# Optimization experiments

Measured on AMD Instinct MI355X. Metric: run time of the kernel, lower is better.

The kernel has to match this reference:

```python
import jax, jax.numpy as jnp
import numpy as np
from jax import lax

FEAT_STRIDE = 16
SCALES = np.array([8.0, 16.0, 32.0])
RATIOS = np.array([0.5, 1.0, 2.0])
PRE_NMS_TOPN = 6000
POST_NMS_TOPN = 300
NMS_THRESH = 0.7


def _whctrs(a):
    w = a[2] - a[0] + 1.0
    h = a[3] - a[1] + 1.0
    return w, h, a[0] + 0.5 * (w - 1.0), a[1] + 0.5 * (h - 1.0)


def _mkanchors(ws, hs, xc, yc):
    return np.stack([xc - 0.5 * (ws - 1.0), yc - 0.5 * (hs - 1.0),
                     xc + 0.5 * (ws - 1.0), yc + 0.5 * (hs - 1.0)], axis=1)


def generate_anchors(base_size=16):
    base = np.array([0.0, 0.0, base_size - 1.0, base_size - 1.0])
    w, h, xc, yc = _whctrs(base)
    size = w * h
    ws = np.round(np.sqrt(size / RATIOS))
    hs = np.round(ws * RATIOS)
    ratio_anchors = _mkanchors(ws, hs, np.full_like(ws, xc), np.full_like(ws, yc))
    out = []
    for a in ratio_anchors:
        w, h, xc, yc = _whctrs(a)
        out.append(_mkanchors(w * SCALES, h * SCALES,
                              np.full_like(SCALES, xc), np.full_like(SCALES, yc)))
    return np.concatenate(out, axis=0).astype(np.float32)  # (A=9, 4)


def _pairwise_iou(boxes):
    x1, y1, x2, y2 = boxes[:, 0], boxes[:, 1], boxes[:, 2], boxes[:, 3]
    area = (x2 - x1 + 1.0) * (y2 - y1 + 1.0)
    iw = jnp.maximum(0.0, jnp.minimum(x2[:, None], x2[None, :]) - jnp.maximum(x1[:, None], x1[None, :]) + 1.0)
    ih = jnp.maximum(0.0, jnp.minimum(y2[:, None], y2[None, :]) - jnp.maximum(y1[:, None], y1[None, :]) + 1.0)
    inter = iw * ih
    return inter / (area[:, None] + area[None, :] - inter)


def _nms_keep(iou, thresh):
    n = iou.shape[0]
    idx = jnp.arange(n)
    def body(keep, i):
        suppress = keep[i] & (iou[i] > thresh) & (idx > i)
        return keep & (~suppress), None
    keep, _ = lax.scan(body, jnp.ones((n,), dtype=bool), idx)
    return keep


def _per_image(props, sc):
    # descending score sort, keep top pre_nms
    order = jnp.argsort(-sc)[:PRE_NMS_TOPN]
    boxes = props[order]  # (PRE, 4)
    iou = _pairwise_iou(boxes)  # (PRE, PRE)
    keep = _nms_keep(iou, NMS_THRESH)
    rank = jnp.cumsum(keep) - 1
    valid = keep & (rank < POST_NMS_TOPN)
    slot = jnp.where(valid, rank, POST_NMS_TOPN)  # dump invalid into spare slot
    out = jnp.zeros((POST_NMS_TOPN + 1, 4), boxes.dtype)
    out = out.at[slot].set(jnp.where(valid[:, None], boxes, 0.0))
    return out[:POST_NMS_TOPN]


def reference(scores, bbox_deltas, im_info):
    B, C2, H, W = scores.shape
    A = C2 // 2
    anchors = jnp.asarray(generate_anchors())  # (A, 4)
    sx = (jnp.arange(W) * FEAT_STRIDE).astype(jnp.float32)
    sy = (jnp.arange(H) * FEAT_STRIDE).astype(jnp.float32)
    gy, gx = jnp.meshgrid(sy, sx, indexing='ij')
    shifts = jnp.stack([gx.ravel(), gy.ravel(), gx.ravel(), gy.ravel()], axis=1)  # (K, 4)
    all_anchors = (anchors[None, :, :] + shifts[:, None, :]).reshape(-1, 4)  # (K*A, 4)

    deltas = bbox_deltas.transpose(0, 2, 3, 1).reshape(B, -1, 4)  # (B, K*A, 4)
    sc = scores[:, A:].transpose(0, 2, 3, 1).reshape(B, -1)        # (B, K*A)

    # bbox_transform_inv
    wa = all_anchors[:, 2] - all_anchors[:, 0] + 1.0
    ha = all_anchors[:, 3] - all_anchors[:, 1] + 1.0
    cxa = all_anchors[:, 0] + 0.5 * wa
    cya = all_anchors[:, 1] + 0.5 * ha
    dx, dy, dw, dh = deltas[..., 0], deltas[..., 1], deltas[..., 2], deltas[..., 3]
    pcx = dx * wa + cxa
    pcy = dy * ha + cya
    pw = jnp.exp(dw) * wa
    ph = jnp.exp(dh) * ha
    x1 = pcx - 0.5 * pw
    y1 = pcy - 0.5 * ph
    x2 = pcx + 0.5 * pw
    y2 = pcy + 0.5 * ph

    # clip_boxes
    im_h = im_info[:, 0:1]
    im_w = im_info[:, 1:2]
    x1 = jnp.clip(x1, 0.0, im_w - 1.0)
    x2 = jnp.clip(x2, 0.0, im_w - 1.0)
    y1 = jnp.clip(y1, 0.0, im_h - 1.0)
    y2 = jnp.clip(y2, 0.0, im_h - 1.0)
    props = jnp.stack([x1, y1, x2, y2], axis=-1)  # (B, K*A, 4)

    out_boxes = jax.vmap(_per_image)(props, sc)  # (B, POST, 4)
    batch_idx = jnp.broadcast_to(
        jnp.arange(B, dtype=out_boxes.dtype)[:, None, None], (B, POST_NMS_TOPN, 1))
    return jnp.concatenate([batch_idx, out_boxes], axis=-1)  # (B, POST, 5)


def setup_inputs() -> dict:
    key = jax.random.key(0)
    k1, k2 = jax.random.split(key)
    B, A, H, W = 4, 9, 50, 76
    scores = jax.random.uniform(k1, (B, 2 * A, H, W), dtype=jnp.float32)
    bbox_deltas = jax.random.normal(k2, (B, 4 * A, H, W), dtype=jnp.float32) * 0.1
    im_info = jnp.ones((B, 3), jnp.float32) * jnp.array([800.0, 1216.0, 1.0], jnp.float32)
    return {"scores": scores, "bbox_deltas": bbox_deltas, "im_info": im_info}
```

## Files before the change

kernel.cpp:

```cpp
#include <hip/hip_runtime.h>
#include <stdint.h>

#define B_     4
#define A_     9
#define H_     50
#define W_     76
#define HW_    (H_ * W_)
#define N_     (HW_ * A_)
#define PRE_   6000
#define POST_  300
#define NBIN   16384
#define BINOFF 0xC000
#define SKCAP  8192
#define ACTMAX 256
#define FXCAP  2048
#define NB_    94

__constant__ float c_anchors[9][4] = {
    { -84.f,  -40.f,  99.f,  55.f},
    {-176.f,  -88.f, 191.f, 103.f},
    {-360.f, -184.f, 375.f, 199.f},
    { -56.f,  -56.f,  71.f,  71.f},
    {-120.f, -120.f, 135.f, 135.f},
    {-248.f, -248.f, 263.f, 263.f},
    { -36.f,  -80.f,  51.f,  95.f},
    { -80.f, -168.f,  95.f, 183.f},
    {-168.f, -344.f, 183.f, 359.f},
};

__device__ __forceinline__ int sb_bin(unsigned int sb) {
    int bin = (int)((~sb) >> 16) - BINOFF;
    return bin < 0 ? 0 : bin;
}

__global__ __launch_bounds__(1024) void k_hp(const float* __restrict__ scores,
                                             unsigned int* __restrict__ hist,
                                             unsigned int* __restrict__ prefw,
                                             unsigned int* __restrict__ actA,
                                             unsigned int* __restrict__ actB,
                                             unsigned int* __restrict__ actcnt) {
    int b = blockIdx.x, tid = threadIdx.x;
    int lane = tid & 63, wid = tid >> 6;
    __shared__ unsigned int s_hist[NBIN];
    __shared__ unsigned int s_ws[64];
    __shared__ unsigned int s_aA[ACTMAX];
    __shared__ unsigned int s_aB[ACTMAX];
    __shared__ int s_actn;
    if (tid == 0) s_actn = 0;
    for (int i = tid; i < NBIN; i += 1024) s_hist[i] = 0u;
    __syncthreads();

    const float* sc = scores + (size_t)((b * 2 * A_) + A_) * HW_;
    for (int i = tid; i < N_; i += 1024) {
        unsigned int sb = __float_as_uint(sc[i]);
        atomicAdd(&s_hist[sb_bin(sb)], 1u);
    }
    __syncthreads();

    uint4* h4 = (uint4*)(hist + b * NBIN);
    uint4* p4 = (uint4*)(prefw + b * NBIN);
    const uint4* s4 = (const uint4*)s_hist;
    uint4 c[4];
    unsigned int tsum[4], inc[4];
#pragma unroll
    for (int p = 0; p < 4; ++p) {
        c[p] = s4[p * 1024 + tid];
        tsum[p] = c[p].x + c[p].y + c[p].z + c[p].w;
        unsigned int v = tsum[p];
#pragma unroll
        for (int off = 1; off < 64; off <<= 1) {
            unsigned int t = __shfl_up(v, off);
            if (lane >= off) v += t;
        }
        inc[p] = v;
        if (lane == 63) s_ws[p * 16 + wid] = v;
    }
    __syncthreads();
    if (wid == 0) {
        unsigned int v = s_ws[lane];
        unsigned int s = v;
#pragma unroll
        for (int off = 1; off < 64; off <<= 1) {
            unsigned int t = __shfl_up(s, off);
            if (lane >= off) s += t;
        }
        s_ws[lane] = s - v;
    }
    __syncthreads();
#pragma unroll
    for (int p = 0; p < 4; ++p) {
        unsigned int base = s_ws[p * 16 + wid] + inc[p] - tsum[p];
        uint4 r;
        r.x = base;
        r.y = base + c[p].x;
        r.z = r.y + c[p].y;
        r.w = r.z + c[p].z;
        h4[p * 1024 + tid] = r;
        p4[p * 1024 + tid] = r;
        unsigned int cc[4] = {c[p].x, c[p].y, c[p].z, c[p].w};
        unsigned int rr[4] = {r.x, r.y, r.z, r.w};
        int bin0 = (p * 1024 + tid) * 4;
#pragma unroll
        for (int q = 0; q < 4; ++q) {
            if (cc[q] > 0 && rr[q] < (unsigned int)PRE_) {
                int pos = atomicAdd(&s_actn, 1);
                if (pos < ACTMAX) {
                    s_aA[pos] = rr[q];
                    s_aB[pos] = ((unsigned int)(bin0 + q) << 16) | (cc[q] & 0xffffu);
                }
            }
        }
    }
    __syncthreads();
    int n = s_actn; if (n > ACTMAX) n = ACTMAX;
    for (int i = tid; i < n; i += 1024) {
        actA[b * ACTMAX + i] = s_aA[i];
        actB[b * ACTMAX + i] = s_aB[i];
    }
    if (tid == 0) actcnt[b] = (unsigned int)n;
}

__global__ void k_scatter(const float* __restrict__ scores,
                          const unsigned int* __restrict__ hist,
                          unsigned int* __restrict__ prefw,
                          unsigned long long* __restrict__ skeys) {
    int b = blockIdx.y;
    int i = blockIdx.x * 256 + threadIdx.x;
    if (i >= N_) return;
    const float* sc = scores + (size_t)((b * 2 * A_) + A_) * HW_;
    unsigned int sb = __float_as_uint(sc[i]);
    int bin = sb_bin(sb);
    if (hist[b * NBIN + bin] < (unsigned int)PRE_) {
        unsigned int slot = atomicAdd(&prefw[b * NBIN + bin], 1u);
        if (slot < SKCAP) {
            int a = i / HW_, r = i - a * HW_;
            unsigned int n = (unsigned int)(r * A_ + a);
            skeys[b * SKCAP + slot] =
                (((unsigned long long)(~sb)) << 32) | (unsigned long long)n;
        }
    }
}

__device__ __forceinline__ void compute_box(int b, unsigned int n,
                                            const float* __restrict__ deltas,
                                            const float* __restrict__ im_info,
                                            float box[4]) {
#pragma clang fp contract(off)
    int a   = (int)(n % A_);
    int pos = (int)(n / A_);
    int w   = pos % W_;
    int h   = pos / W_;
    float a0 = c_anchors[a][0] + (float)(w * 16);
    float a1 = c_anchors[a][1] + (float)(h * 16);
    float a2 = c_anchors[a][2] + (float)(w * 16);
    float a3 = c_anchors[a][3] + (float)(h * 16);
    float wa  = a2 - a0 + 1.f;
    float ha  = a3 - a1 + 1.f;
    float cxa = a0 + 0.5f * wa;
    float cya = a1 + 0.5f * ha;
    int base = ((b * 4 * A_ + a * 4) * H_ + h) * W_ + w;
    const int chs = HW_;
    float dx = deltas[base];
    float dy = deltas[base + chs];
    float dw = deltas[base + 2 * chs];
    float dh = deltas[base + 3 * chs];
    float pcx = dx * wa + cxa;
    float pcy = dy * ha + cya;
    float pw  = expf(dw) * wa;
    float ph  = expf(dh) * ha;
    float x1 = pcx - 0.5f * pw;
    float y1 = pcy - 0.5f * ph;
    float x2 = pcx + 0.5f * pw;
    float y2 = pcy + 0.5f * ph;
    float imh = im_info[b * 3 + 0], imw = im_info[b * 3 + 1];
    x1 = fminf(fmaxf(x1, 0.f), imw - 1.f);
    x2 = fminf(fmaxf(x2, 0.f), imw - 1.f);
    y1 = fminf(fmaxf(y1, 0.f), imh - 1.f);
    y2 = fminf(fmaxf(y2, 0.f), imh - 1.f);
    box[0] = x1; box[1] = y1; box[2] = x2; box[3] = y2;
}

__global__ __launch_bounds__(256) void k_fixup(const unsigned long long* __restrict__ skeys,
                                               const unsigned int* __restrict__ actA,
                                               const unsigned int* __restrict__ actB,
                                               const unsigned int* __restrict__ actcnt,
                                               const float* __restrict__ deltas,
                                               const float* __restrict__ im_info,
                                               float* __restrict__ sboxes) {
    int b = blockIdx.y;
    unsigned int nact = actcnt[b];
    if (nact > ACTMAX) nact = ACTMAX;
    if (blockIdx.x >= nact) return;
    int tid = threadIdx.x;
    unsigned int start = actA[b * ACTMAX + blockIdx.x];
    unsigned int ab    = actB[b * ACTMAX + blockIdx.x];
    unsigned int cnt   = ab & 0xffffu;
    unsigned int m = cnt;
    if (start + m > SKCAP) m = SKCAP - start;
    if (m > FXCAP) m = FXCAP;
    __shared__ unsigned long long lk[FXCAP];
    for (unsigned int i = tid; i < m; i += 256) lk[i] = skeys[b * SKCAP + start + i];
    __syncthreads();
    float4* sb4 = (float4*)sboxes;
    for (unsigned int e = tid; e < m; e += 256) {
        unsigned long long k = lk[e];
        unsigned int r = 0;
        for (unsigned int i = 0; i < m; ++i) r += (lk[i] < k) ? 1u : 0u;
        unsigned int pos = start + r;
        if (pos < (unsigned int)PRE_) {
            unsigned int n = (unsigned int)(k & 0xffffffffull);
            float box[4];
            compute_box(b, n, deltas, im_info, box);
            sb4[b * PRE_ + pos] = make_float4(box[0], box[1], box[2], box[3]);
        }
    }
}

__device__ __forceinline__ bool iou_gt(float4 p, float pa, float4 q, float qa) {
    float iw = fminf(p.z, q.z) - fmaxf(p.x, q.x) + 1.f;
    float ih = fminf(p.w, q.w) - fmaxf(p.y, q.y) + 1.f;
    iw = fmaxf(iw, 0.f); ih = fmaxf(ih, 0.f);
    float inter = iw * ih;
    float iou = inter / ((pa + qa) - inter);
    return iou > 0.7f;
}

__global__ __launch_bounds__(64) void k_mask(const float* __restrict__ sboxes,
                                             unsigned long long* __restrict__ mask) {
    int b = blockIdx.y, blk = blockIdx.x;
    int lane = threadIdx.x;
    const float4* bb = (const float4*)sboxes + b * PRE_;
    int idx = blk * 64 + lane;
    float4 v = bb[idx < PRE_ ? idx : PRE_ - 1];
    float area = ((v.z - v.x) + 1.f) * ((v.w - v.y) + 1.f);
    unsigned long long myrow = 0ull;
    for (int i = 0; i < 64; ++i) {
        float4 p;
        p.x = __shfl(v.x, i); p.y = __shfl(v.y, i);
        p.z = __shfl(v.z, i); p.w = __shfl(v.w, i);
        float pa = __shfl(area, i);
        unsigned long long bal = __ballot((lane > i) && iou_gt(p, pa, v, area));
        if (lane == i) myrow = bal;
    }
    mask[(b * NB_ + blk) * 64 + lane] = myrow;
}

__global__ __launch_bounds__(1024) void k_nms(const float* __restrict__ sboxes,
                                              const unsigned long long* __restrict__ mask,
                                              float* __restrict__ out) {
    int b = blockIdx.x;
    int tid = threadIdx.x;
    int lane = tid & 63;
    int wave = tid >> 6;
    __shared__ float4 s_box[POST_ + 64];
    __shared__ float  s_ar [POST_ + 64];
    __shared__ unsigned long long s_pend[2][16];
    __shared__ int s_cnt[2];
    __shared__ int s_final;
    if (tid < 32) ((unsigned long long*)s_pend)[tid] = 0ull;
    if (tid < 2) s_cnt[tid] = 0;
    if (tid == 0) s_final = 0;
    __syncthreads();

    const float4* bb = (const float4*)sboxes + b * PRE_;
    float* ob = out + b * POST_ * 5;

    float4 vme;
    unsigned long long rowme = 0ull;
    if (wave == 0) {
        vme = bb[lane];
        rowme = mask[(b * NB_ + 0) * 64 + lane];
    } else {
        vme = bb[64 + lane];
    }

    for (int k = 0; k < NB_; ++k) {
        int Cm1 = s_cnt[(k + 1) & 1];
        if (Cm1 >= POST_) break;
        if (wave == 0) {
            int idx = k * 64 + lane;
            bool valid = idx < PRE_;
            float4 v = vme;
            unsigned long long row = rowme;
            if (k + 1 < NB_) {
                int nidx = (k + 1) * 64 + lane;
                vme = bb[nidx < PRE_ ? nidx : PRE_ - 1];
                rowme = mask[(b * NB_ + k + 1) * 64 + lane];
            }
            float area = ((v.z - v.x) + 1.f) * ((v.w - v.y) + 1.f);
            int Cm2 = s_cnt[k & 1];
            bool sup = !valid;
            int kk = Cm2;
            for (; kk + 1 < Cm1; kk += 2) {
                float4 k0 = s_box[kk],   k1 = s_box[kk + 1];
                float  r0 = s_ar [kk],   r1 = s_ar [kk + 1];
                sup = sup | iou_gt(v, area, k0, r0) | iou_gt(v, area, k1, r1);
            }
            for (; kk < Cm1; ++kk)
                sup = sup | iou_gt(v, area, s_box[kk], s_ar[kk]);
            unsigned long long supm = __ballot(sup);
            const unsigned long long* pnd = s_pend[k & 1];
#pragma unroll
            for (int w2 = 1; w2 < 16; ++w2) supm |= pnd[w2];
            unsigned int rlo = (unsigned int)row;
            unsigned int rhi = (unsigned int)(row >> 32);
            unsigned long long alive = ~supm;
            unsigned long long keepm = 0ull;
            while (alive) {
                int i = __builtin_ctzll(alive);
                keepm |= (1ull << i);
                alive &= ~(1ull << i);
                unsigned long long mlo = (unsigned int)__builtin_amdgcn_readlane((int)rlo, i);
                unsigned long long mhi = (unsigned int)__builtin_amdgcn_readlane((int)rhi, i);
                alive &= ~((mhi << 32) | mlo);
            }
            if ((keepm >> lane) & 1ull) {
                int my = Cm1 + __builtin_popcountll(keepm & ((1ull << lane) - 1ull));
                s_box[my] = v;
                s_ar [my] = area;
                if (my < POST_) {
                    ob[my * 5 + 0] = (float)b;
                    ob[my * 5 + 1] = v.x; ob[my * 5 + 2] = v.y;
                    ob[my * 5 + 3] = v.z; ob[my * 5 + 4] = v.w;
                }
            }
            if (lane == 0) {
                int nc = Cm1 + __builtin_popcountll(keepm);
                s_cnt[k & 1] = nc;
                s_final = nc;
            }
        } else if (k + 1 < NB_) {
            int jdx = (k + 1) * 64 + lane;
            bool valid2 = jdx < PRE_;
            float4 v2 = vme;
            if (k + 2 < NB_) {
                int nj = (k + 2) * 64 + lane;
                vme = bb[nj < PRE_ ? nj : PRE_ - 1];
            }
            float area2 = ((v2.z - v2.x) + 1.f) * ((v2.w - v2.y) + 1.f);
            bool sup2 = !valid2;
            int kk = wave - 1;
            for (; kk + 45 < Cm1; kk += 60) {
                float4 k0 = s_box[kk],      k1 = s_box[kk + 15];
                float4 k2 = s_box[kk + 30], k3 = s_box[kk + 45];
                float  r0 = s_ar [kk],      r1 = s_ar [kk + 15];
                float  r2 = s_ar [kk + 30], r3 = s_ar [kk + 45];
                sup2 = sup2 | iou_gt(v2, area2, k0, r0) | iou_gt(v2, area2, k1, r1)
                            | iou_gt(v2, area2, k2, r2) | iou_gt(v2, area2, k3, r3);
            }
            for (; kk < Cm1; kk += 15)
                sup2 = sup2 | iou_gt(v2, area2, s_box[kk], s_ar[kk]);
            unsigned long long bal = __ballot(sup2);
            if (lane == 0) s_pend[(k + 1) & 1][wave] = bal;
        }
        __syncthreads();
    }
    __syncthreads();
    int kept = s_final;
    int start = kept < POST_ ? kept : POST_;
    for (int r = start + tid; r < POST_; r += 1024) {
        ob[r * 5 + 0] = (float)b;
        ob[r * 5 + 1] = 0.f; ob[r * 5 + 2] = 0.f;
        ob[r * 5 + 3] = 0.f; ob[r * 5 + 4] = 0.f;
    }
}

extern "C" void kernel_launch(void* const* d_in, const int* in_sizes, int n_in,
                              void* d_out, int out_size, void* d_ws, size_t ws_size,
                              hipStream_t stream) {
    const float* scores  = (const float*)d_in[0];
    const float* deltas  = (const float*)d_in[1];
    const float* im_info = (const float*)d_in[2];
    float* out = (float*)d_out;

    char* ws = (char*)d_ws;
    unsigned int*       hist    = (unsigned int*)      (ws);
    unsigned long long* maskb   = (unsigned long long*)(ws);
    unsigned int*       prefw   = (unsigned int*)      (ws + 262144);
    unsigned long long* skeys   = (unsigned long long*)(ws + 524288);
    unsigned int*       actA    = (unsigned int*)      (ws + 786432);
    unsigned int*       actB    = (unsigned int*)      (ws + 790528);
    unsigned int*       actcnt  = (unsigned int*)      (ws + 794624);
    float*              sbx     = (float*)             (ws + 794656);

    k_hp<<<B_, 1024, 0, stream>>>(scores, hist, prefw, actA, actB, actcnt);
    dim3 g2d((N_ + 255) / 256, B_);
    k_scatter<<<g2d, 256, 0, stream>>>(scores, hist, prefw, skeys);
    dim3 fgrid(ACTMAX, B_);
    k_fixup<<<fgrid, 256, 0, stream>>>(skeys, actA, actB, actcnt, deltas, im_info, sbx);
    dim3 mgrid(NB_, B_);
    k_mask<<<mgrid, 64, 0, stream>>>(sbx, maskb);
    k_nms<<<B_, 1024, 0, stream>>>(sbx, maskb, out);
}
```

Measured before the change: 90.44 us.

## Fuse histogram with scatter and compute NMS mask tiles inside NMS kernel

Merges the histogram/prefix kernel with the scatter kernel, so the scan offsets stay in shared memory and a separate launch plus global hist/prefw arrays go away. It also drops the separate mask kernel: the NMS kernel now builds the 64x64 intra-block suppression tiles itself and computes the tile for block k+2 during iteration k in a 3-slot shared ring. This removes two launches and a global mask round-trip. The cost is that scatter now runs on only B blocks instead of a wide grid, and extra IoU work sits inside the serial NMS loop.

```diff
diff --git a/kernel.cpp b/kernel.cpp
--- a/kernel.cpp
+++ b/kernel.cpp
@@ -33,112 +33,87 @@
     return bin < 0 ? 0 : bin;
 }
 
-__global__ __launch_bounds__(1024) void k_hp(const float* __restrict__ scores,
-                                             unsigned int* __restrict__ hist,
-                                             unsigned int* __restrict__ prefw,
-                                             unsigned int* __restrict__ actA,
-                                             unsigned int* __restrict__ actB,
-                                             unsigned int* __restrict__ actcnt) {
-    int b = blockIdx.x, tid = threadIdx.x;
-    int lane = tid & 63, wid = tid >> 6;
-    __shared__ unsigned int s_hist[NBIN];
-    __shared__ unsigned int s_ws[64];
+__global__ __launch_bounds__(1024) void k_hps(const float* __restrict__ scores,
+                                              unsigned long long* __restrict__ skeys,
+                                              unsigned int* __restrict__ actA,
+                                              unsigned int* __restrict__ actB,
+                                              unsigned int* __restrict__ actcnt) {
+    const int b = blockIdx.x, tid = threadIdx.x;
+    const int lane = tid & 63, wid = tid >> 6;
+    __shared__ unsigned int LHIST[NBIN];
+    __shared__ unsigned int s_wsum[16];
     __shared__ unsigned int s_aA[ACTMAX];
     __shared__ unsigned int s_aB[ACTMAX];
-    __shared__ int s_actn;
-    if (tid == 0) s_actn = 0;
-    for (int i = tid; i < NBIN; i += 1024) s_hist[i] = 0u;
+    __shared__ int s_actn, s_binhi;
+
+    for (int i = tid; i < NBIN; i += 1024) LHIST[i] = 0u;
+    if (tid == 0) { s_actn = 0; s_binhi = 0; }
     __syncthreads();
 
     const float* sc = scores + (size_t)((b * 2 * A_) + A_) * HW_;
     for (int i = tid; i < N_; i += 1024) {
         unsigned int sb = __float_as_uint(sc[i]);
-        atomicAdd(&s_hist[sb_bin(sb)], 1u);
-    }
-    __syncthreads();
-
-    uint4* h4 = (uint4*)(hist + b * NBIN);
-    uint4* p4 = (uint4*)(prefw + b * NBIN);
-    const uint4* s4 = (const uint4*)s_hist;
-    uint4 c[4];
-    unsigned int tsum[4], inc[4];
-#pragma unroll
-    for (int p = 0; p < 4; ++p) {
-        c[p] = s4[p * 1024 + tid];
-        tsum[p] = c[p].x + c[p].y + c[p].z + c[p].w;
-        unsigned int v = tsum[p];
+        atomicAdd(&LHIST[sb_bin(sb)], 1u);
+    }
+    __syncthreads();
+
+    {
+        int base0 = tid * 16;
+        unsigned int sum = 0;
+        for (int q = 0; q < 16; ++q) sum += LHIST[base0 + q];
+        unsigned int inc = sum;
 #pragma unroll
         for (int off = 1; off < 64; off <<= 1) {
-            unsigned int t = __shfl_up(v, off);
-            if (lane >= off) v += t;
-        }
-        inc[p] = v;
-        if (lane == 63) s_ws[p * 16 + wid] = v;
-    }
-    __syncthreads();
-    if (wid == 0) {
-        unsigned int v = s_ws[lane];
-        unsigned int s = v;
-#pragma unroll
-        for (int off = 1; off < 64; off <<= 1) {
-            unsigned int t = __shfl_up(s, off);
-            if (lane >= off) s += t;
-        }
-        s_ws[lane] = s - v;
-    }
-    __syncthreads();
-#pragma unroll
-    for (int p = 0; p < 4; ++p) {
-        unsigned int base = s_ws[p * 16 + wid] + inc[p] - tsum[p];
-        uint4 r;
-        r.x = base;
-        r.y = base + c[p].x;
-        r.z = r.y + c[p].y;
-        r.w = r.z + c[p].z;
-        h4[p * 1024 + tid] = r;
-        p4[p * 1024 + tid] = r;
-        unsigned int cc[4] = {c[p].x, c[p].y, c[p].z, c[p].w};
-        unsigned int rr[4] = {r.x, r.y, r.z, r.w};
-        int bin0 = (p * 1024 + tid) * 4;
-#pragma unroll
-        for (int q = 0; q < 4; ++q) {
-            if (cc[q] > 0 && rr[q] < (unsigned int)PRE_) {
-                int pos = atomicAdd(&s_actn, 1);
-                if (pos < ACTMAX) {
-                    s_aA[pos] = rr[q];
-                    s_aB[pos] = ((unsigned int)(bin0 + q) << 16) | (cc[q] & 0xffffu);
+            unsigned int t = __shfl_up(inc, off);
+            if (lane >= off) inc += t;
+        }
+        if (lane == 63) s_wsum[wid] = inc;
+        __syncthreads();
+        unsigned int wbase = 0;
+        for (int wq = 0; wq < wid; ++wq) wbase += s_wsum[wq];
+        unsigned int run = wbase + inc - sum;
+        int mybinhi = -1;
+        for (int q = 0; q < 16; ++q) {
+            unsigned int c = LHIST[base0 + q];
+            LHIST[base0 + q] = run;
+            if (run < (unsigned int)PRE_) {
+                mybinhi = base0 + q;
+                if (c > 0) {
+                    int pos = atomicAdd(&s_actn, 1);
+                    if (pos < ACTMAX) {
+                        s_aA[pos] = run;
+                        s_aB[pos] = ((unsigned int)(base0 + q) << 16) | (c & 0xffffu);
+                    }
                 }
             }
-        }
-    }
-    __syncthreads();
+            run += c;
+        }
+        if (mybinhi >= 0) atomicMax(&s_binhi, mybinhi);
+    }
+    __syncthreads();
+
+    {
+        int binhi = s_binhi;
+        for (int i = tid; i < N_; i += 1024) {
+            unsigned int sb = __float_as_uint(sc[i]);
+            int bin = sb_bin(sb);
+            if (bin <= binhi) {
+                unsigned int slot = atomicAdd(&LHIST[bin], 1u);
+                if (slot < SKCAP) {
+                    int a = i / HW_, r = i - a * HW_;
+                    unsigned int n = (unsigned int)(r * A_ + a);
+                    skeys[b * SKCAP + slot] =
+                        (((unsigned long long)(~sb)) << 32) | (unsigned long long)n;
+                }
+            }
+        }
+    }
     int n = s_actn; if (n > ACTMAX) n = ACTMAX;
     for (int i = tid; i < n; i += 1024) {
         actA[b * ACTMAX + i] = s_aA[i];
         actB[b * ACTMAX + i] = s_aB[i];
     }
     if (tid == 0) actcnt[b] = (unsigned int)n;
-}
-
-__global__ void k_scatter(const float* __restrict__ scores,
-                          const unsigned int* __restrict__ hist,
-                          unsigned int* __restrict__ prefw,
-                          unsigned long long* __restrict__ skeys) {
-    int b = blockIdx.y;
-    int i = blockIdx.x * 256 + threadIdx.x;
-    if (i >= N_) return;
-    const float* sc = scores + (size_t)((b * 2 * A_) + A_) * HW_;
-    unsigned int sb = __float_as_uint(sc[i]);
-    int bin = sb_bin(sb);
-    if (hist[b * NBIN + bin] < (unsigned int)PRE_) {
-        unsigned int slot = atomicAdd(&prefw[b * NBIN + bin], 1u);
-        if (slot < SKCAP) {
-            int a = i / HW_, r = i - a * HW_;
-            unsigned int n = (unsigned int)(r * A_ + a);
-            skeys[b * SKCAP + slot] =
-                (((unsigned long long)(~sb)) << 32) | (unsigned long long)n;
-        }
-    }
 }
 
 __device__ __forceinline__ void compute_box(int b, unsigned int n,
@@ -225,28 +200,7 @@
     return iou > 0.7f;
 }
 
-__global__ __launch_bounds__(64) void k_mask(const float* __restrict__ sboxes,
-                                             unsigned long long* __restrict__ mask) {
-    int b = blockIdx.y, blk = blockIdx.x;
-    int lane = threadIdx.x;
-    const float4* bb = (const float4*)sboxes + b * PRE_;
-    int idx = blk * 64 + lane;
-    float4 v = bb[idx < PRE_ ? idx : PRE_ - 1];
-    float area = ((v.z - v.x) + 1.f) * ((v.w - v.y) + 1.f);
-    unsigned long long myrow = 0ull;
-    for (int i = 0; i < 64; ++i) {
-        float4 p;
-        p.x = __shfl(v.x, i); p.y = __shfl(v.y, i);
-        p.z = __shfl(v.z, i); p.w = __shfl(v.w, i);
-        float pa = __shfl(area, i);
-        unsigned long long bal = __ballot((lane > i) && iou_gt(p, pa, v, area));
-        if (lane == i) myrow = bal;
-    }
-    mask[(b * NB_ + blk) * 64 + lane] = myrow;
-}
-
 __global__ __launch_bounds__(1024) void k_nms(const float* __restrict__ sboxes,
-                                              const unsigned long long* __restrict__ mask,
                                               float* __restrict__ out) {
     int b = blockIdx.x;
     int tid = threadIdx.x;
@@ -255,24 +209,34 @@
     __shared__ float4 s_box[POST_ + 64];
     __shared__ float  s_ar [POST_ + 64];
     __shared__ unsigned long long s_pend[2][16];
+    __shared__ unsigned long long s_mtile[3][64];
     __shared__ int s_cnt[2];
     __shared__ int s_final;
     if (tid < 32) ((unsigned long long*)s_pend)[tid] = 0ull;
     if (tid < 2) s_cnt[tid] = 0;
     if (tid == 0) s_final = 0;
-    __syncthreads();
 
     const float4* bb = (const float4*)sboxes + b * PRE_;
     float* ob = out + b * POST_ * 5;
 
+    {
+        int blk01 = (wave < 8) ? 0 : 1;
+        int wrel = wave & 7;
+        float4 vb = bb[blk01 * 64 + lane];
+        float ab = ((vb.z - vb.x) + 1.f) * ((vb.w - vb.y) + 1.f);
+        for (int r = wrel * 8; r < wrel * 8 + 8; ++r) {
+            float4 p;
+            p.x = __shfl(vb.x, r); p.y = __shfl(vb.y, r);
+            p.z = __shfl(vb.z, r); p.w = __shfl(vb.w, r);
+            float pa = __shfl(ab, r);
+            unsigned long long bal = __ballot((lane > r) && iou_gt(p, pa, vb, ab));
+            if (lane == 0) s_mtile[blk01][r] = bal;
+        }
+    }
     float4 vme;
-    unsigned long long rowme = 0ull;
-    if (wave == 0) {
-        vme = bb[lane];
-        rowme = mask[(b * NB_ + 0) * 64 + lane];
-    } else {
-        vme = bb[64 + lane];
-    }
+    if (wave == 0) vme = bb[lane];
+    else           vme = bb[64 + lane];
+    __syncthreads();
 
     for (int k = 0; k < NB_; ++k) {
         int Cm1 = s_cnt[(k + 1) & 1];
@@ -281,11 +245,10 @@
             int idx = k * 64 + lane;
             bool valid = idx < PRE_;
             float4 v = vme;
-            unsigned long long row = rowme;
+            unsigned long long row = s_mtile[k % 3][lane];
             if (k + 1 < NB_) {
                 int nidx = (k + 1) * 64 + lane;
                 vme = bb[nidx < PRE_ ? nidx : PRE_ - 1];
-                rowme = mask[(b * NB_ + k + 1) * 64 + lane];
             }
             float area = ((v.z - v.x) + 1.f) * ((v.w - v.y) + 1.f);
             int Cm2 = s_cnt[k & 1];
@@ -352,6 +315,18 @@
                 sup2 = sup2 | iou_gt(v2, area2, s_box[kk], s_ar[kk]);
             unsigned long long bal = __ballot(sup2);
             if (lane == 0) s_pend[(k + 1) & 1][wave] = bal;
+            if (k + 2 < NB_) {
+                float amex = ((vme.z - vme.x) + 1.f) * ((vme.w - vme.y) + 1.f);
+                int slot = (k + 2) % 3;
+                for (int r = wave - 1; r < 64; r += 15) {
+                    float4 p;
+                    p.x = __shfl(vme.x, r); p.y = __shfl(vme.y, r);
+                    p.z = __shfl(vme.z, r); p.w = __shfl(vme.w, r);
+                    float pa = __shfl(amex, r);
+                    unsigned long long mb = __ballot((lane > r) && iou_gt(p, pa, vme, amex));
+                    if (lane == 0) s_mtile[slot][r] = mb;
+                }
+            }
         }
         __syncthreads();
     }
@@ -374,21 +349,14 @@
     float* out = (float*)d_out;
 
     char* ws = (char*)d_ws;
-    unsigned int*       hist    = (unsigned int*)      (ws);
-    unsigned long long* maskb   = (unsigned long long*)(ws);
-    unsigned int*       prefw   = (unsigned int*)      (ws + 262144);
-    unsigned long long* skeys   = (unsigned long long*)(ws + 524288);
-    unsigned int*       actA    = (unsigned int*)      (ws + 786432);
-    unsigned int*       actB    = (unsigned int*)      (ws + 790528);
-    unsigned int*       actcnt  = (unsigned int*)      (ws + 794624);
-    float*              sbx     = (float*)             (ws + 794656);
-
-    k_hp<<<B_, 1024, 0, stream>>>(scores, hist, prefw, actA, actB, actcnt);
-    dim3 g2d((N_ + 255) / 256, B_);
-    k_scatter<<<g2d, 256, 0, stream>>>(scores, hist, prefw, skeys);
+    unsigned long long* skeys  = (unsigned long long*)(ws);
+    unsigned int*       actA   = (unsigned int*)      (ws + 262144);
+    unsigned int*       actB   = (unsigned int*)      (ws + 266240);
+    unsigned int*       actcnt = (unsigned int*)      (ws + 270336);
+    float*              sbx    = (float*)             (ws + 270368);
+
+    k_hps<<<B_, 1024, 0, stream>>>(scores, skeys, actA, actB, actcnt);
     dim3 fgrid(ACTMAX, B_);
     k_fixup<<<fgrid, 256, 0, stream>>>(skeys, actA, actB, actcnt, deltas, im_info, sbx);
-    dim3 mgrid(NB_, B_);
-    k_mask<<<mgrid, 64, 0, stream>>>(sbx, maskb);
-    k_nms<<<B_, 1024, 0, stream>>>(sbx, maskb, out);
-}
+    k_nms<<<B_, 1024, 0, stream>>>(sbx, out);
+}
```

Result: faster. 81.74 us (-9.6%).
